# Optimization experiments

Hardware: AMD Instinct MI355X
Metric: run time of the kernel (lower is better)

## Reference

```python
import jax, jax.numpy as jnp
import numpy as np

N = 50000
E = 1600000
IN_DIM = 256
HID = 128
EPS = 1e-5


def _bn(x, gamma, beta):
    # BatchNorm1d forward in training mode: biased batch stats
    mean = jnp.mean(x, axis=0)
    var = jnp.mean((x - mean) ** 2, axis=0)
    return (x - mean) * jax.lax.rsqrt(var + EPS) * gamma + beta


def _sage(x, edge_index, Wl, bl, Wr):
    # PyG SAGEConv with mean aggregation:
    #   out = lin_l(mean_{j in N(i)} x_j) + lin_r(x_i)
    src, dst = edge_index[0], edge_index[1]
    agg = jax.ops.segment_sum(x[src], dst, num_segments=N)          # [N, H]
    cnt = jax.ops.segment_sum(jnp.ones((src.shape[0],), x.dtype), dst, num_segments=N)
    mean = agg / jnp.maximum(cnt, 1.0)[:, None]
    return mean @ Wl + bl + x @ Wr


def setup_inputs() -> dict:
    key = jax.random.key(0)
    ks = jax.random.split(key, 16)
    s_in = 1.0 / np.sqrt(IN_DIM)
    s_h = 1.0 / np.sqrt(HID)
    return {
        "x": jax.random.normal(ks[0], (N, IN_DIM), jnp.float32),
        "edge_index": jax.random.randint(ks[1], (2, E), 0, N, jnp.int32),
        # input_linear: Linear(IN_DIM, HID) + BN
        "W_in": jax.random.uniform(ks[2], (IN_DIM, HID), jnp.float32, -s_in, s_in),
        "b_in": jax.random.uniform(ks[3], (HID,), jnp.float32, -s_in, s_in),
        "g1": jnp.ones((HID,), jnp.float32), "be1": jnp.zeros((HID,), jnp.float32),
        # hidden_linear: Linear(HID, HID) + BN
        "W_hid": jax.random.uniform(ks[4], (HID, HID), jnp.float32, -s_h, s_h),
        "b_hid": jax.random.uniform(ks[5], (HID,), jnp.float32, -s_h, s_h),
        "g2": jnp.ones((HID,), jnp.float32), "be2": jnp.zeros((HID,), jnp.float32),
        # graph_conv1: SAGEConv(HID, HID) + BN
        "Wl1": jax.random.uniform(ks[6], (HID, HID), jnp.float32, -s_h, s_h),
        "bl1": jax.random.uniform(ks[7], (HID,), jnp.float32, -s_h, s_h),
        "Wr1": jax.random.uniform(ks[8], (HID, HID), jnp.float32, -s_h, s_h),
        "g3": jnp.ones((HID,), jnp.float32), "be3": jnp.zeros((HID,), jnp.float32),
        # graph_conv2: SAGEConv(HID, HID) + BN
        "Wl2": jax.random.uniform(ks[9], (HID, HID), jnp.float32, -s_h, s_h),
        "bl2": jax.random.uniform(ks[10], (HID,), jnp.float32, -s_h, s_h),
        "Wr2": jax.random.uniform(ks[11], (HID, HID), jnp.float32, -s_h, s_h),
        "g4": jnp.ones((HID,), jnp.float32), "be4": jnp.zeros((HID,), jnp.float32),
    }


def reference(x, edge_index, W_in, b_in, g1, be1, W_hid, b_hid, g2, be2,
              Wl1, bl1, Wr1, g3, be3, Wl2, bl2, Wr2, g4, be4):
    feat = jax.nn.relu(_bn(x @ W_in + b_in, g1, be1))
    feat = jax.nn.relu(_bn(feat @ W_hid + b_hid, g2, be2))
    out = _bn(_sage(feat, edge_index, Wl1, bl1, Wr1), g3, be3)
    out = _bn(_sage(out, edge_index, Wl2, bl2, Wr2), g4, be4)
    return (feat, out)
```

## Files before the change

kernel.cpp:

```cpp
#include <hip/hip_runtime.h>
#include <stdint.h>

#define NN 50000
#define EE 1600000
#define IN_DIMC 256
#define HIDC 128
#define EPSC 1e-5f

#define NB 196
#define GA 512
#define CHUNK 3125

typedef unsigned short ushort_t;
typedef __attribute__((ext_vector_type(8))) short short8;
typedef __attribute__((ext_vector_type(4))) float floatx4;

static __device__ inline ushort_t f2bf(float f) {
    unsigned int u = __float_as_uint(f);
    u = u + 0x7fffu + ((u >> 16) & 1u);
    return (ushort_t)(u >> 16);
}
static __device__ inline unsigned int pack2(float a, float b) {
    return (unsigned int)f2bf(a) | ((unsigned int)f2bf(b) << 16);
}
static __device__ inline float bf2f(unsigned int bits16) {
    return __uint_as_float(bits16 << 16);
}

__global__ __launch_bounds__(256) void tcvt_all_kernel(
    const float* __restrict__ W_in, const float* __restrict__ W_hid,
    const float* __restrict__ Wl1, const float* __restrict__ Wr1,
    const float* __restrict__ Wl2, const float* __restrict__ Wr2,
    ushort_t* __restrict__ Wt_in, ushort_t* __restrict__ Wt_hid,
    ushort_t* __restrict__ Wtl1, ushort_t* __restrict__ Wtr1,
    ushort_t* __restrict__ Wtl2, ushort_t* __restrict__ Wtr2)
{
    const int idx = blockIdx.x * 256 + threadIdx.x;
    if (idx < 32768) {
        const int n = idx >> 8;
        const int k = idx & 255;
        Wt_in[idx] = f2bf(W_in[(size_t)k * 128 + n]);
    } else if (idx < 32768 + 5 * 16384) {
        const int r = idx - 32768;
        const int seg = r / 16384;
        const int j = r - seg * 16384;
        const int n = j >> 7;
        const int k = j & 127;
        const float* W; ushort_t* Wt;
        switch (seg) {
            case 0: W = W_hid; Wt = Wt_hid; break;
            case 1: W = Wl1;  Wt = Wtl1;  break;
            case 2: W = Wr1;  Wt = Wtr1;  break;
            case 3: W = Wl2;  Wt = Wtl2;  break;
            default: W = Wr2; Wt = Wtr2;  break;
        }
        Wt[j] = f2bf(W[(size_t)k * 128 + n]);
    }
}

__global__ __launch_bounds__(256) void mfma_gemm_kernel(
    const void* __restrict__ A1, const ushort_t* __restrict__ Wt1, int K1, int a1type,
    const void* __restrict__ A2, const ushort_t* __restrict__ Wt2, int K2,
    const float* __restrict__ bias, float* __restrict__ C, int M,
    const float* __restrict__ preStats, const float* __restrict__ preG,
    const float* __restrict__ preBe, float* __restrict__ outStats)
{
    __shared__ ushort_t As[64 * 72];
    __shared__ ushort_t Bs[128 * 72];
    __shared__ float aArr[128], bArr[128];
    __shared__ float red_s[4][64], red_q[4][64];

    const int t     = threadIdx.x;
    const int lane  = t & 63;
    const int wave  = t >> 6;
    const int quad  = lane >> 4;
    const int l15   = lane & 15;
    const int mhalf = wave & 1;
    const int nhalf = wave >> 1;
    const int row0  = blockIdx.x * 64;
    const int doAffine = (preStats != nullptr);

    if (doAffine && t < 128) {
        const float invM = 1.0f / (float)M;
        const float mean = preStats[t] * invM;
        float var = preStats[128 + t] * invM - mean * mean;
        if (var < 0.0f) var = 0.0f;
        const float s = preG[t] / sqrtf(var + EPSC);
        aArr[t] = s;
        bArr[t] = preBe[t] - mean * s;
    }
    if (doAffine) __syncthreads();

    floatx4 acc[2][4];
    #pragma unroll
    for (int i = 0; i < 2; i++)
        #pragma unroll
        for (int j = 0; j < 4; j++)
            acc[i][j] = (floatx4){0.0f, 0.0f, 0.0f, 0.0f};

    for (int s = 0; s < 2; s++) {
        const void*     A     = s ? A2  : A1;
        const ushort_t* Wt    = s ? Wt2 : Wt1;
        const int       K     = s ? K2  : K1;
        const int       atype = s ? 1   : a1type;
        if (A == nullptr) continue;

        for (int kc = 0; kc < K; kc += 64) {
            #pragma unroll
            for (int p = 0; p < 2; p++) {
                const int idx = p * 256 + t;
                const int r   = idx >> 3;
                const int c0  = (idx & 7) * 8;
                int gr = row0 + r;
                if (gr > M - 1) gr = M - 1;
                if (atype == 0) {
                    const float* Af = (const float*)A;
                    const size_t base = (size_t)gr * K + kc + c0;
                    float4 v0 = *(const float4*)(Af + base);
                    float4 v1 = *(const float4*)(Af + base + 4);
                    if (doAffine && s == 0) {
                        const int k0 = kc + c0;
                        v0.x = fmaxf(aArr[k0]     * v0.x + bArr[k0],     0.0f);
                        v0.y = fmaxf(aArr[k0 + 1] * v0.y + bArr[k0 + 1], 0.0f);
                        v0.z = fmaxf(aArr[k0 + 2] * v0.z + bArr[k0 + 2], 0.0f);
                        v0.w = fmaxf(aArr[k0 + 3] * v0.w + bArr[k0 + 3], 0.0f);
                        v1.x = fmaxf(aArr[k0 + 4] * v1.x + bArr[k0 + 4], 0.0f);
                        v1.y = fmaxf(aArr[k0 + 5] * v1.y + bArr[k0 + 5], 0.0f);
                        v1.z = fmaxf(aArr[k0 + 6] * v1.z + bArr[k0 + 6], 0.0f);
                        v1.w = fmaxf(aArr[k0 + 7] * v1.w + bArr[k0 + 7], 0.0f);
                    }
                    uint4 w;
                    w.x = pack2(v0.x, v0.y);
                    w.y = pack2(v0.z, v0.w);
                    w.z = pack2(v1.x, v1.y);
                    w.w = pack2(v1.z, v1.w);
                    *(uint4*)(As + r * 72 + c0) = w;
                } else {
                    const ushort_t* Ab = (const ushort_t*)A;
                    *(uint4*)(As + r * 72 + c0) =
                        *(const uint4*)(Ab + (size_t)gr * K + kc + c0);
                }
            }
            #pragma unroll
            for (int p = 0; p < 4; p++) {
                const int idx = p * 256 + t;
                const int n   = idx >> 3;
                const int c0  = (idx & 7) * 8;
                *(uint4*)(Bs + n * 72 + c0) =
                    *(const uint4*)(Wt + (size_t)n * K + kc + c0);
            }
            __syncthreads();

            #pragma unroll
            for (int ks = 0; ks < 2; ks++) {
                const int ko = ks * 32 + quad * 8;
                const short8 a0 = *(const short8*)(As + (mhalf * 32 + l15) * 72 + ko);
                const short8 a1 = *(const short8*)(As + (mhalf * 32 + 16 + l15) * 72 + ko);
                short8 b[4];
                #pragma unroll
                for (int j = 0; j < 4; j++)
                    b[j] = *(const short8*)(Bs + (nhalf * 64 + j * 16 + l15) * 72 + ko);
                #pragma unroll
                for (int j = 0; j < 4; j++) {
                    acc[0][j] = __builtin_amdgcn_mfma_f32_16x16x32_bf16(a0, b[j], acc[0][j], 0, 0, 0);
                    acc[1][j] = __builtin_amdgcn_mfma_f32_16x16x32_bf16(a1, b[j], acc[1][j], 0, 0, 0);
                }
            }
            __syncthreads();
        }
    }

    float s_[4], q_[4];
    #pragma unroll
    for (int j = 0; j < 4; j++) { s_[j] = 0.0f; q_[j] = 0.0f; }

    #pragma unroll
    for (int j = 0; j < 4; j++) {
        const int col = nhalf * 64 + j * 16 + l15;
        const float bv = bias[col];
        #pragma unroll
        for (int i = 0; i < 2; i++) {
            const int rbase = row0 + mhalf * 32 + i * 16 + quad * 4;
            #pragma unroll
            for (int reg = 0; reg < 4; reg++) {
                const float val = acc[i][j][reg] + bv;
                const int r_ = rbase + reg;
                if (r_ < M) {
                    C[(size_t)r_ * HIDC + col] = val;
                    s_[j] += val;
                    q_[j] += val * val;
                }
            }
        }
    }
    #pragma unroll
    for (int j = 0; j < 4; j++) {
        s_[j] += __shfl_xor(s_[j], 16, 64);
        s_[j] += __shfl_xor(s_[j], 32, 64);
        q_[j] += __shfl_xor(q_[j], 16, 64);
        q_[j] += __shfl_xor(q_[j], 32, 64);
    }
    if (quad == 0) {
        #pragma unroll
        for (int j = 0; j < 4; j++) {
            red_s[wave][j * 16 + l15] = s_[j];
            red_q[wave][j * 16 + l15] = q_[j];
        }
    }
    __syncthreads();
    if (t < 128) {
        const int c = t;
        const int g = c >> 6;
        const int cc = c & 63;
        const float S = red_s[g * 2][cc] + red_s[g * 2 + 1][cc];
        const float Q = red_q[g * 2][cc] + red_q[g * 2 + 1][cc];
        atomicAdd(&outStats[c], S);
        atomicAdd(&outStats[128 + c], Q);
    }
}

__global__ __launch_bounds__(256) void bn_apply_kernel(
    const float* __restrict__ src, float* __restrict__ dstF,
    ushort_t* __restrict__ dstB, const float* __restrict__ stats,
    const float* __restrict__ gamma, const float* __restrict__ beta,
    int relu, int M)
{
    __shared__ float sc[128], sh[128];
    const int t = threadIdx.x;
    if (t < 128) {
        const float invM = 1.0f / (float)M;
        const float mean = stats[t] * invM;
        float var = stats[128 + t] * invM - mean * mean;
        if (var < 0.0f) var = 0.0f;
        const float s = gamma[t] / sqrtf(var + EPSC);
        sc[t] = s;
        sh[t] = beta[t] - mean * s;
    }
    __syncthreads();

    const int total4 = M * HIDC / 4;
    for (int i = blockIdx.x * 256 + t; i < total4; i += gridDim.x * 256) {
        float4 v = ((const float4*)src)[i];
        const int c = (i * 4) & 127;
        v.x = v.x * sc[c]     + sh[c];
        v.y = v.y * sc[c + 1] + sh[c + 1];
        v.z = v.z * sc[c + 2] + sh[c + 2];
        v.w = v.w * sc[c + 3] + sh[c + 3];
        if (relu) {
            v.x = fmaxf(v.x, 0.0f); v.y = fmaxf(v.y, 0.0f);
            v.z = fmaxf(v.z, 0.0f); v.w = fmaxf(v.w, 0.0f);
        }
        if (dstF) ((float4*)dstF)[i] = v;
        if (dstB) {
            uint2 w;
            w.x = pack2(v.x, v.y);
            w.y = pack2(v.z, v.w);
            *(uint2*)(dstB + (size_t)i * 4) = w;
        }
    }
}

__global__ __launch_bounds__(256) void bucket_hist_kernel(
    const int* __restrict__ dstArr, int* __restrict__ hist2D)
{
    __shared__ int hist[NB];
    const int t = threadIdx.x;
    for (int i = t; i < NB; i += 256) hist[i] = 0;
    __syncthreads();
    const int e0 = blockIdx.x * CHUNK;
    const int e1 = e0 + CHUNK;
    for (int e = e0 + t; e < e1; e += 256)
        atomicAdd(&hist[dstArr[e] >> 8], 1);
    __syncthreads();
    for (int i = t; i < NB; i += 256)
        hist2D[(size_t)i * GA + blockIdx.x] = hist[i];
}

__global__ __launch_bounds__(256) void bucket_offsets_kernel(
    int* __restrict__ hist2D, int* __restrict__ bucketBase, int* __restrict__ rowp)
{
    __shared__ int wtot[4];
    const int t = threadIdx.x;
    int tot = 0;
    if (t < NB) {
        int4* p = (int4*)(hist2D + (size_t)t * GA);
        int s = 0;
        for (int i = 0; i < GA / 4; i++) {
            int4 h = p[i];
            int4 o;
            o.x = s; s += h.x;
            o.y = s; s += h.y;
            o.z = s; s += h.z;
            o.w = s; s += h.w;
            p[i] = o;
        }
        tot = s;
    }
    const int lane = t & 63, w = t >> 6;
    int x = tot;
    #pragma unroll
    for (int off = 1; off < 64; off <<= 1) {
        const int y = __shfl_up(x, off);
        if (lane >= off) x += y;
    }
    if (lane == 63) wtot[w] = x;
    __syncthreads();
    int woff = 0;
    #pragma unroll
    for (int j = 0; j < 4; j++) if (j < w) woff += wtot[j];
    const int excl = x + woff - tot;
    if (t < NB) bucketBase[t] = excl;
    if (t == 0) { bucketBase[NB] = EE; rowp[NN] = EE; }
}

__global__ __launch_bounds__(256) void bucket_scatter_kernel(
    const int* __restrict__ srcArr, const int* __restrict__ dstArr,
    const int* __restrict__ hist2D, const int* __restrict__ bucketBase,
    int2* __restrict__ ebuf)
{
    __shared__ int cur[NB];
    const int t = threadIdx.x;
    for (int i = t; i < NB; i += 256)
        cur[i] = bucketBase[i] + hist2D[(size_t)i * GA + blockIdx.x];
    __syncthreads();
    const int e0 = blockIdx.x * CHUNK;
    const int e1 = e0 + CHUNK;
    for (int e = e0 + t; e < e1; e += 256) {
        const int d = dstArr[e];
        const int s = srcArr[e];
        const int p = atomicAdd(&cur[d >> 8], 1);
        ebuf[p] = make_int2(s, d);
    }
}

__global__ __launch_bounds__(256) void fine_sort_kernel(
    const int2* __restrict__ ebuf, const int* __restrict__ bucketBase,
    int* __restrict__ rowp, int* __restrict__ col)
{
    __shared__ int cnt[256];
    __shared__ int wtot[4];
    const int b = blockIdx.x;
    const int t = threadIdx.x;
    const int bb0 = bucketBase[b];
    const int bb1 = bucketBase[b + 1];
    cnt[t] = 0;
    __syncthreads();
    for (int e = bb0 + t; e < bb1; e += 256)
        atomicAdd(&cnt[ebuf[e].y & 255], 1);
    __syncthreads();
    const int lane = t & 63, w = t >> 6;
    const int v = cnt[t];
    int x = v;
    #pragma unroll
    for (int off = 1; off < 64; off <<= 1) {
        const int y = __shfl_up(x, off);
        if (lane >= off) x += y;
    }
    if (lane == 63) wtot[w] = x;
    __syncthreads();
    int woff = 0;
    #pragma unroll
    for (int j = 0; j < 4; j++) if (j < w) woff += wtot[j];
    const int excl = x + woff - v;
    const int node = b * 256 + t;
    if (node < NN) rowp[node] = bb0 + excl;
    __syncthreads();
    cnt[t] = excl;
    __syncthreads();
    for (int e = bb0 + t; e < bb1; e += 256) {
        const int2 sd = ebuf[e];
        const int p = atomicAdd(&cnt[sd.y & 255], 1);
        col[bb0 + p] = sd.x;
    }
}

__global__ __launch_bounds__(256) void agg_kernel(
    const ushort_t* __restrict__ F, const int* __restrict__ row_ptr,
    const int* __restrict__ col, ushort_t* __restrict__ Mout)
{
    const int lane = threadIdx.x & 63;
    const int wave = blockIdx.x * (blockDim.x >> 6) + (threadIdx.x >> 6);
    const int nwaves = gridDim.x * (blockDim.x >> 6);
    const int coff = lane * 2;

    for (int n = wave; n < NN; n += nwaves) {
        const int b = __builtin_amdgcn_readfirstlane(row_ptr[n]);
        const int e = __builtin_amdgcn_readfirstlane(row_ptr[n + 1]);
        const int deg = e - b;
        float accx = 0.0f, accy = 0.0f;
        int j = b;
        for (; j + 8 <= e; j += 8) {
            const int s0 = col[j + 0];
            const int s1 = col[j + 1];
            const int s2 = col[j + 2];
            const int s3 = col[j + 3];
            const int s4 = col[j + 4];
            const int s5 = col[j + 5];
            const int s6 = col[j + 6];
            const int s7 = col[j + 7];
            const unsigned int v0 = *(const unsigned int*)(F + (size_t)s0 * HIDC + coff);
            const unsigned int v1 = *(const unsigned int*)(F + (size_t)s1 * HIDC + coff);
            const unsigned int v2 = *(const unsigned int*)(F + (size_t)s2 * HIDC + coff);
            const unsigned int v3 = *(const unsigned int*)(F + (size_t)s3 * HIDC + coff);
            const unsigned int v4 = *(const unsigned int*)(F + (size_t)s4 * HIDC + coff);
            const unsigned int v5 = *(const unsigned int*)(F + (size_t)s5 * HIDC + coff);
            const unsigned int v6 = *(const unsigned int*)(F + (size_t)s6 * HIDC + coff);
            const unsigned int v7 = *(const unsigned int*)(F + (size_t)s7 * HIDC + coff);
            accx += bf2f(v0 & 0xffffu) + bf2f(v1 & 0xffffu) + bf2f(v2 & 0xffffu)
                  + bf2f(v3 & 0xffffu) + bf2f(v4 & 0xffffu) + bf2f(v5 & 0xffffu)
                  + bf2f(v6 & 0xffffu) + bf2f(v7 & 0xffffu);
            accy += bf2f(v0 >> 16) + bf2f(v1 >> 16) + bf2f(v2 >> 16)
                  + bf2f(v3 >> 16) + bf2f(v4 >> 16) + bf2f(v5 >> 16)
                  + bf2f(v6 >> 16) + bf2f(v7 >> 16);
        }
        for (; j < e; j++) {
            const int s = col[j];
            const unsigned int v = *(const unsigned int*)(F + (size_t)s * HIDC + coff);
            accx += bf2f(v & 0xffffu);
            accy += bf2f(v >> 16);
        }
        const float inv = 1.0f / (float)(deg > 1 ? deg : 1);
        *(unsigned int*)(Mout + (size_t)n * HIDC + coff) =
            pack2(accx * inv, accy * inv);
    }
}

extern "C" void kernel_launch(void* const* d_in, const int* in_sizes, int n_in,
                              void* d_out, int out_size, void* d_ws, size_t ws_size,
                              hipStream_t stream)
{
    const float* x     = (const float*)d_in[0];
    const int*   ei    = (const int*)  d_in[1];
    const float* W_in  = (const float*)d_in[2];
    const float* b_in  = (const float*)d_in[3];
    const float* g1    = (const float*)d_in[4];
    const float* be1   = (const float*)d_in[5];
    const float* W_hid = (const float*)d_in[6];
    const float* b_hid = (const float*)d_in[7];
    const float* g2    = (const float*)d_in[8];
    const float* be2   = (const float*)d_in[9];
    const float* Wl1   = (const float*)d_in[10];
    const float* bl1   = (const float*)d_in[11];
    const float* Wr1   = (const float*)d_in[12];
    const float* g3    = (const float*)d_in[13];
    const float* be3   = (const float*)d_in[14];
    const float* Wl2   = (const float*)d_in[15];
    const float* bl2   = (const float*)d_in[16];
    const float* Wr2   = (const float*)d_in[17];
    const float* g4    = (const float*)d_in[18];
    const float* be4   = (const float*)d_in[19];

    const int* srcArr = ei;
    const int* dstArr = ei + EE;

    char* ws = (char*)d_ws;
    float*    bufA      = (float*)ws;    ws += (size_t)NN * HIDC * sizeof(float);
    float*    bufB      = (float*)ws;    ws += (size_t)NN * HIDC * sizeof(float);
    ushort_t* featB16   = (ushort_t*)ws; ws += (size_t)NN * HIDC * sizeof(ushort_t);
    ushort_t* o3B16     = (ushort_t*)ws; ws += (size_t)NN * HIDC * sizeof(ushort_t);
    ushort_t* aggB16    = (ushort_t*)ws; ws += (size_t)NN * HIDC * sizeof(ushort_t);
    float*    stats     = (float*)ws;    ws += 4 * 256 * sizeof(float);
    int*      hist2D    = (int*)ws;      ws += (size_t)NB * GA * sizeof(int);
    int*      bucketBase= (int*)ws;      ws += (NB + 4) * sizeof(int);
    int*      rowp      = (int*)ws;      ws += (size_t)(NN + 4) * sizeof(int);
    int*      colIdx    = (int*)ws;      ws += (size_t)EE * sizeof(int);
    int2*     ebuf      = (int2*)ws;     ws += (size_t)EE * sizeof(int2);
    ushort_t* Wt_in     = (ushort_t*)ws; ws += 128 * 256 * sizeof(ushort_t);
    ushort_t* Wt_hid    = (ushort_t*)ws; ws += 128 * 128 * sizeof(ushort_t);
    ushort_t* Wtl1      = (ushort_t*)ws; ws += 128 * 128 * sizeof(ushort_t);
    ushort_t* Wtr1      = (ushort_t*)ws; ws += 128 * 128 * sizeof(ushort_t);
    ushort_t* Wtl2      = (ushort_t*)ws; ws += 128 * 128 * sizeof(ushort_t);
    ushort_t* Wtr2      = (ushort_t*)ws; ws += 128 * 128 * sizeof(ushort_t);

    float* out0 = (float*)d_out;
    float* out1 = out0 + (size_t)NN * HIDC;

    hipMemsetAsync(stats, 0, 4 * 256 * sizeof(float), stream);

    tcvt_all_kernel<<<448, 256, 0, stream>>>(W_in, W_hid, Wl1, Wr1, Wl2, Wr2,
                                             Wt_in, Wt_hid, Wtl1, Wtr1, Wtl2, Wtr2);

    bucket_hist_kernel<<<GA, 256, 0, stream>>>(dstArr, hist2D);
    bucket_offsets_kernel<<<1, 256, 0, stream>>>(hist2D, bucketBase, rowp);
    bucket_scatter_kernel<<<GA, 256, 0, stream>>>(srcArr, dstArr, hist2D,
                                                  bucketBase, ebuf);
    fine_sort_kernel<<<NB, 256, 0, stream>>>(ebuf, bucketBase, rowp, colIdx);

    const int gemmGrid = (NN + 63) / 64;

    mfma_gemm_kernel<<<gemmGrid, 256, 0, stream>>>(
        x, Wt_in, IN_DIMC, 0, nullptr, nullptr, 0,
        b_in, bufA, NN, nullptr, nullptr, nullptr, stats + 0);

    mfma_gemm_kernel<<<gemmGrid, 256, 0, stream>>>(
        bufA, Wt_hid, HIDC, 0, nullptr, nullptr, 0,
        b_hid, bufB, NN, stats + 0, g1, be1, stats + 256);

    bn_apply_kernel<<<1024, 256, 0, stream>>>(bufB, out0, featB16,
                                              stats + 256, g2, be2, 1, NN);

    agg_kernel<<<4096, 256, 0, stream>>>(featB16, rowp, colIdx, aggB16);
    mfma_gemm_kernel<<<gemmGrid, 256, 0, stream>>>(
        aggB16, Wtl1, HIDC, 1, featB16, Wtr1, HIDC,
        bl1, bufA, NN, nullptr, nullptr, nullptr, stats + 512);

    bn_apply_kernel<<<1024, 256, 0, stream>>>(bufA, nullptr, o3B16,
                                              stats + 512, g3, be3, 0, NN);

    agg_kernel<<<4096, 256, 0, stream>>>(o3B16, rowp, colIdx, aggB16);
    mfma_gemm_kernel<<<gemmGrid, 256, 0, stream>>>(
        aggB16, Wtl2, HIDC, 1, o3B16, Wtr2, HIDC,
        bl2, bufB, NN, nullptr, nullptr, nullptr, stats + 768);

    bn_apply_kernel<<<1024, 256, 0, stream>>>(bufB, out1, nullptr,
                                              stats + 768, g4, be4, 0, NN);
}
```

Baseline: 467.5 us.

## Load GEMM A fragments directly to registers and enlarge tile to 128 rows

The MFMA GEMM now gives each wave 32 rows by all 128 columns. A operands are loaded straight from global memory into register fragments, so the shared-memory A tile and its sync are gone. The K chunk grows from 64 to 128 and the block tile from 64 to 128 rows, which halves the grid and stages only B in LDS. Register pressure rises with 64 accumulator floats plus 8 A fragments per thread, which may cut occupancy. Global A loads are also less coalesced, since each lane reads a 16-byte piece of a different row.

```diff
diff --git a/kernel.cpp b/kernel.cpp
--- a/kernel.cpp
+++ b/kernel.cpp
@@ -65,19 +65,16 @@
     const float* __restrict__ preStats, const float* __restrict__ preG,
     const float* __restrict__ preBe, float* __restrict__ outStats)
 {
-    __shared__ ushort_t As[64 * 72];
-    __shared__ ushort_t Bs[128 * 72];
-    __shared__ float aArr[128], bArr[128];
-    __shared__ float red_s[4][64], red_q[4][64];
-
-    const int t     = threadIdx.x;
-    const int lane  = t & 63;
-    const int wave  = t >> 6;
-    const int quad  = lane >> 4;
-    const int l15   = lane & 15;
-    const int mhalf = wave & 1;
-    const int nhalf = wave >> 1;
-    const int row0  = blockIdx.x * 64;
+    __shared__ ushort_t Bs[128 * 136];
+    __shared__ __align__(16) float aArr[128], bArr[128];
+    __shared__ float red_s[4][128], red_q[4][128];
+
+    const int t    = threadIdx.x;
+    const int lane = t & 63;
+    const int wave = t >> 6;
+    const int quad = lane >> 4;
+    const int l15  = lane & 15;
+    const int row0 = blockIdx.x * 128 + wave * 32;
     const int doAffine = (preStats != nullptr);
 
     if (doAffine && t < 128) {
@@ -91,12 +88,15 @@
     }
     if (doAffine) __syncthreads();
 
-    floatx4 acc[2][4];
+    floatx4 acc[2][8];
     #pragma unroll
     for (int i = 0; i < 2; i++)
         #pragma unroll
-        for (int j = 0; j < 4; j++)
+        for (int j = 0; j < 8; j++)
             acc[i][j] = (floatx4){0.0f, 0.0f, 0.0f, 0.0f};
+
+    const int ksq = quad * 8;
+    bool firstChunk = true;
 
     for (int s = 0; s < 2; s++) {
         const void*     A     = s ? A2  : A1;
@@ -105,85 +105,100 @@
         const int       atype = s ? 1   : a1type;
         if (A == nullptr) continue;
 
-        for (int kc = 0; kc < K; kc += 64) {
+        for (int kc = 0; kc < K; kc += 128) {
+            if (!firstChunk) __syncthreads();
+            firstChunk = false;
+
             #pragma unroll
-            for (int p = 0; p < 2; p++) {
+            for (int p = 0; p < 8; p++) {
                 const int idx = p * 256 + t;
-                const int r   = idx >> 3;
-                const int c0  = (idx & 7) * 8;
-                int gr = row0 + r;
-                if (gr > M - 1) gr = M - 1;
-                if (atype == 0) {
-                    const float* Af = (const float*)A;
-                    const size_t base = (size_t)gr * K + kc + c0;
-                    float4 v0 = *(const float4*)(Af + base);
-                    float4 v1 = *(const float4*)(Af + base + 4);
-                    if (doAffine && s == 0) {
-                        const int k0 = kc + c0;
-                        v0.x = fmaxf(aArr[k0]     * v0.x + bArr[k0],     0.0f);
-                        v0.y = fmaxf(aArr[k0 + 1] * v0.y + bArr[k0 + 1], 0.0f);
-                        v0.z = fmaxf(aArr[k0 + 2] * v0.z + bArr[k0 + 2], 0.0f);
-                        v0.w = fmaxf(aArr[k0 + 3] * v0.w + bArr[k0 + 3], 0.0f);
-                        v1.x = fmaxf(aArr[k0 + 4] * v1.x + bArr[k0 + 4], 0.0f);
-                        v1.y = fmaxf(aArr[k0 + 5] * v1.y + bArr[k0 + 5], 0.0f);
-                        v1.z = fmaxf(aArr[k0 + 6] * v1.z + bArr[k0 + 6], 0.0f);
-                        v1.w = fmaxf(aArr[k0 + 7] * v1.w + bArr[k0 + 7], 0.0f);
-                    }
-                    uint4 w;
-                    w.x = pack2(v0.x, v0.y);
-                    w.y = pack2(v0.z, v0.w);
-                    w.z = pack2(v1.x, v1.y);
-                    w.w = pack2(v1.z, v1.w);
-                    *(uint4*)(As + r * 72 + c0) = w;
-                } else {
-                    const ushort_t* Ab = (const ushort_t*)A;
-                    *(uint4*)(As + r * 72 + c0) =
-                        *(const uint4*)(Ab + (size_t)gr * K + kc + c0);
-                }
-            }
-            #pragma unroll
-            for (int p = 0; p < 4; p++) {
-                const int idx = p * 256 + t;
-                const int n   = idx >> 3;
-                const int c0  = (idx & 7) * 8;
-                *(uint4*)(Bs + n * 72 + c0) =
+                const int n   = idx >> 4;
+                const int c0  = (idx & 15) * 8;
+                *(uint4*)(Bs + n * 136 + c0) =
                     *(const uint4*)(Wt + (size_t)n * K + kc + c0);
             }
             __syncthreads();
 
-            #pragma unroll
-            for (int ks = 0; ks < 2; ks++) {
-                const int ko = ks * 32 + quad * 8;
-                const short8 a0 = *(const short8*)(As + (mhalf * 32 + l15) * 72 + ko);
-                const short8 a1 = *(const short8*)(As + (mhalf * 32 + 16 + l15) * 72 + ko);
-                short8 b[4];
+            short8 afrag[2][4];
+            if (atype == 1) {
+                const ushort_t* Ab = (const ushort_t*)A;
                 #pragma unroll
-                for (int j = 0; j < 4; j++)
-                    b[j] = *(const short8*)(Bs + (nhalf * 64 + j * 16 + l15) * 72 + ko);
+                for (int mt = 0; mt < 2; mt++) {
+                    int gr = row0 + mt * 16 + l15;
+                    if (gr > M - 1) gr = M - 1;
+                    const size_t base = (size_t)gr * K + kc + ksq;
+                    #pragma unroll
+                    for (int ks = 0; ks < 4; ks++)
+                        afrag[mt][ks] = *(const short8*)(Ab + base + ks * 32);
+                }
+            } else {
+                const float* Af = (const float*)A;
                 #pragma unroll
-                for (int j = 0; j < 4; j++) {
-                    acc[0][j] = __builtin_amdgcn_mfma_f32_16x16x32_bf16(a0, b[j], acc[0][j], 0, 0, 0);
-                    acc[1][j] = __builtin_amdgcn_mfma_f32_16x16x32_bf16(a1, b[j], acc[1][j], 0, 0, 0);
+                for (int mt = 0; mt < 2; mt++) {
+                    int gr = row0 + mt * 16 + l15;
+                    if (gr > M - 1) gr = M - 1;
+                    const size_t base = (size_t)gr * K + kc + ksq;
+                    #pragma unroll
+                    for (int ks = 0; ks < 4; ks++) {
+                        float4 v0 = *(const float4*)(Af + base + ks * 32);
+                        float4 v1 = *(const float4*)(Af + base + ks * 32 + 4);
+                        if (doAffine && s == 0) {
+                            const int k0 = ks * 32 + ksq;
+                            const float4 sa0 = *(const float4*)(aArr + k0);
+                            const float4 sb0 = *(const float4*)(bArr + k0);
+                            const float4 sa1 = *(const float4*)(aArr + k0 + 4);
+                            const float4 sb1 = *(const float4*)(bArr + k0 + 4);
+                            v0.x = fmaxf(sa0.x * v0.x + sb0.x, 0.0f);
+                            v0.y = fmaxf(sa0.y * v0.y + sb0.y, 0.0f);
+                            v0.z = fmaxf(sa0.z * v0.z + sb0.z, 0.0f);
+                            v0.w = fmaxf(sa0.w * v0.w + sb0.w, 0.0f);
+                            v1.x = fmaxf(sa1.x * v1.x + sb1.x, 0.0f);
+                            v1.y = fmaxf(sa1.y * v1.y + sb1.y, 0.0f);
+                            v1.z = fmaxf(sa1.z * v1.z + sb1.z, 0.0f);
+                            v1.w = fmaxf(sa1.w * v1.w + sb1.w, 0.0f);
+                        }
+                        uint4 w;
+                        w.x = pack2(v0.x, v0.y);
+                        w.y = pack2(v0.z, v0.w);
+                        w.z = pack2(v1.x, v1.y);
+                        w.w = pack2(v1.z, v1.w);
+                        afrag[mt][ks] = __builtin_bit_cast(short8, w);
+                    }
                 }
             }
-            __syncthreads();
-        }
-    }
-
-    float s_[4], q_[4];
-    #pragma unroll
-    for (int j = 0; j < 4; j++) { s_[j] = 0.0f; q_[j] = 0.0f; }
-
-    #pragma unroll
-    for (int j = 0; j < 4; j++) {
-        const int col = nhalf * 64 + j * 16 + l15;
+
+            #pragma unroll
+            for (int ks = 0; ks < 4; ks++) {
+                const int ko = ks * 32 + ksq;
+                short8 b[8];
+                #pragma unroll
+                for (int j = 0; j < 8; j++)
+                    b[j] = *(const short8*)(Bs + (j * 16 + l15) * 136 + ko);
+                #pragma unroll
+                for (int mt = 0; mt < 2; mt++) {
+                    #pragma unroll
+                    for (int j = 0; j < 8; j++)
+                        acc[mt][j] = __builtin_amdgcn_mfma_f32_16x16x32_bf16(
+                            afrag[mt][ks], b[j], acc[mt][j], 0, 0, 0);
+                }
+            }
+        }
+    }
+
+    float s_[8], q_[8];
+    #pragma unroll
+    for (int j = 0; j < 8; j++) { s_[j] = 0.0f; q_[j] = 0.0f; }
+
+    #pragma unroll
+    for (int j = 0; j < 8; j++) {
+        const int col = j * 16 + l15;
         const float bv = bias[col];
         #pragma unroll
-        for (int i = 0; i < 2; i++) {
-            const int rbase = row0 + mhalf * 32 + i * 16 + quad * 4;
+        for (int mt = 0; mt < 2; mt++) {
+            const int rbase = row0 + mt * 16 + quad * 4;
             #pragma unroll
             for (int reg = 0; reg < 4; reg++) {
-                const float val = acc[i][j][reg] + bv;
+                const float val = acc[mt][j][reg] + bv;
                 const int r_ = rbase + reg;
                 if (r_ < M) {
                     C[(size_t)r_ * HIDC + col] = val;
@@ -194,7 +209,7 @@
         }
     }
     #pragma unroll
-    for (int j = 0; j < 4; j++) {
+    for (int j = 0; j < 8; j++) {
         s_[j] += __shfl_xor(s_[j], 16, 64);
         s_[j] += __shfl_xor(s_[j], 32, 64);
         q_[j] += __shfl_xor(q_[j], 16, 64);
@@ -202,20 +217,17 @@
     }
     if (quad == 0) {
         #pragma unroll
-        for (int j = 0; j < 4; j++) {
+        for (int j = 0; j < 8; j++) {
             red_s[wave][j * 16 + l15] = s_[j];
             red_q[wave][j * 16 + l15] = q_[j];
         }
     }
     __syncthreads();
     if (t < 128) {
-        const int c = t;
-        const int g = c >> 6;
-        const int cc = c & 63;
-        const float S = red_s[g * 2][cc] + red_s[g * 2 + 1][cc];
-        const float Q = red_q[g * 2][cc] + red_q[g * 2 + 1][cc];
-        atomicAdd(&outStats[c], S);
-        atomicAdd(&outStats[128 + c], Q);
+        const float S = red_s[0][t] + red_s[1][t] + red_s[2][t] + red_s[3][t];
+        const float Q = red_q[0][t] + red_q[1][t] + red_q[2][t] + red_q[3][t];
+        atomicAdd(&outStats[t], S);
+        atomicAdd(&outStats[128 + t], Q);
     }
 }
 
@@ -486,7 +498,7 @@
                                                   bucketBase, ebuf);
     fine_sort_kernel<<<NB, 256, 0, stream>>>(ebuf, bucketBase, rowp, colIdx);
 
-    const int gemmGrid = (NN + 63) / 64;
+    const int gemmGrid = (NN + 127) / 128;
 
     mfma_gemm_kernel<<<gemmGrid, 256, 0, stream>>>(
         x, Wt_in, IN_DIMC, 0, nullptr, nullptr, 0,
```

New measurement: 439.4 us. 1.06x faster.
